# Performance work log

Measured on AMD Instinct MI355X. Metric: run time of the kernel, lower is better.

Reference implementation:

```python
import jax, jax.numpy as jnp
import numpy as np

DIM = 512
HEADS = 8
DIM_HEAD = 64
HIDDEN = HEADS * DIM_HEAD  # 512
B, C, H, W = 32, DIM, 32, 32


def setup_inputs() -> dict:
    key = jax.random.key(0)
    ks = jax.random.split(key, 7)
    s_in = 1.0 / np.sqrt(DIM)
    s_h = 1.0 / np.sqrt(HIDDEN)
    x = jax.random.normal(ks[0], (B, C, H, W), dtype=jnp.float32)
    Wq = jax.random.uniform(ks[1], (DIM, HIDDEN), jnp.float32, -s_in, s_in)
    Wk = jax.random.uniform(ks[2], (DIM, HIDDEN), jnp.float32, -s_in, s_in)
    Wv = jax.random.uniform(ks[3], (DIM, HIDDEN), jnp.float32, -s_in, s_in)
    Wp = jax.random.uniform(ks[4], (HIDDEN, DIM), jnp.float32, -s_h, s_h)
    bp = jax.random.uniform(ks[5], (DIM,), jnp.float32, -s_h, s_h)
    return {"x": x, "Wq": Wq, "Wk": Wk, "Wv": Wv, "Wp": Wp, "bp": bp}


def reference(x, Wq, Wk, Wv, Wp, bp):
    b, c, h, w = x.shape
    n = h * w
    xt = x.reshape(b, c, n).transpose(0, 2, 1)  # [B, N, C]
    q = (xt @ Wq).reshape(b, n, HEADS, DIM_HEAD)
    k = (xt @ Wk).reshape(b, n, HEADS, DIM_HEAD)
    v = (xt @ Wv).reshape(b, n, HEADS, DIM_HEAD)
    k_softmax = jax.nn.softmax(k, axis=1)  # softmax over tokens N
    context = jnp.einsum('bnhd,bnhv->bhdv', k_softmax, v)  # [B, H, D, D]
    out = jnp.einsum('bnhd,bhdv->bnhv', q, context).reshape(b, n, HIDDEN)
    out = out @ Wp + bp  # [B, N, C]
    return out.transpose(0, 2, 1).reshape(b, c, h, w)
```

## Files before the change

kernel.cpp:

```cpp
#include <hip/hip_runtime.h>
#include <hip/hip_bf16.h>


__device__ __forceinline__ float bf2f(unsigned short u) {
    union { unsigned int i; float f; } x;
    x.i = ((unsigned int)u) << 16;
    return x.f;
}
__device__ __forceinline__ unsigned short f2bf(float f) {
    unsigned int u = __float_as_uint(f);
    unsigned int lsb = (u >> 16) & 1u;
    u += 0x7fffu + lsb;
    return (unsigned short)(u >> 16);
}
__device__ __forceinline__ float waveReduceMax(float v) {
    #pragma unroll
    for (int off = 32; off > 0; off >>= 1) v = fmaxf(v, __shfl_xor(v, off, 64));
    return v;
}
__device__ __forceinline__ float waveReduceSum(float v) {
    #pragma unroll
    for (int off = 32; off > 0; off >>= 1) v += __shfl_xor(v, off, 64);
    return v;
}

__device__ __forceinline__ void glds16(const unsigned short* g, unsigned short* l) {
    __builtin_amdgcn_global_load_lds(
        (const __attribute__((address_space(1))) unsigned int*)g,
        (__attribute__((address_space(3))) unsigned int*)l,
        16, 0, 0);
}

typedef __bf16 bf16x8 __attribute__((ext_vector_type(8)));
typedef float  f32x4  __attribute__((ext_vector_type(4)));

__global__ void detect_dtype(const unsigned short* __restrict__ x, int* __restrict__ flag)
{
    int t = threadIdx.x;
    unsigned short u = x[2 * t];
    int e = (u >> 7) & 0xFF;
    int sane = (e >= 113 && e <= 142) ? 1 : 0;
    #pragma unroll
    for (int off = 32; off > 0; off >>= 1) sane += __shfl_xor(sane, off, 64);
    if (t == 0) *flag = (sane >= 32) ? 1 : 0;
}

__global__ __launch_bounds__(256) void transpose_x(
    const void* __restrict__ in, unsigned short* __restrict__ out,
    const int* __restrict__ flag)
{
    const int fl = *flag;
    const int b  = blockIdx.z;
    const int c0 = blockIdx.x * 64;
    const int r0 = blockIdx.y * 64;
    __shared__ unsigned short Ts[64][68];
    const int t   = threadIdx.x;
    const int tr  = t >> 4;
    const int tc4 = (t & 15) * 4;
    #pragma unroll
    for (int rr = 0; rr < 4; ++rr) {
        int rl = rr * 16 + tr;
        long off = (long)b * 524288 + (long)(r0 + rl) * 1024 + c0 + tc4;
        unsigned short v[4];
        if (fl) {
            ushort4 u = *(const ushort4*)((const unsigned short*)in + off);
            v[0] = u.x; v[1] = u.y; v[2] = u.z; v[3] = u.w;
        } else {
            float4 u = *(const float4*)((const float*)in + off);
            v[0] = f2bf(u.x); v[1] = f2bf(u.y); v[2] = f2bf(u.z); v[3] = f2bf(u.w);
        }
        #pragma unroll
        for (int q = 0; q < 4; ++q) Ts[tc4 + q][rl] = v[q];
    }
    __syncthreads();
    #pragma unroll
    for (int rr = 0; rr < 4; ++rr) {
        int cl = rr * 16 + tr;
        ushort4 o = *(const ushort4*)&Ts[cl][tc4];
        *(ushort4*)(out + (long)b * 524288 + (long)(c0 + cl) * 512 + r0 + tc4) = o;
    }
}

__global__ __launch_bounds__(256) void transpose_w3(
    const void* __restrict__ w0, const void* __restrict__ w1,
    const void* __restrict__ w2, unsigned short* __restrict__ out,
    const int* __restrict__ flag)
{
    const int fl = *flag;
    const int z  = blockIdx.z;
    const void* in = (z == 0) ? w0 : (z == 1) ? w1 : w2;
    unsigned short* op = out + (long)z * 262144;
    const int c0 = blockIdx.x * 64;
    const int r0 = blockIdx.y * 64;
    __shared__ unsigned short Ts[64][68];
    const int t   = threadIdx.x;
    const int tr  = t >> 4;
    const int tc4 = (t & 15) * 4;
    #pragma unroll
    for (int rr = 0; rr < 4; ++rr) {
        int rl = rr * 16 + tr;
        long off = (long)(r0 + rl) * 512 + c0 + tc4;
        unsigned short v[4];
        if (fl) {
            ushort4 u = *(const ushort4*)((const unsigned short*)in + off);
            v[0] = u.x; v[1] = u.y; v[2] = u.z; v[3] = u.w;
        } else {
            float4 u = *(const float4*)((const float*)in + off);
            v[0] = f2bf(u.x); v[1] = f2bf(u.y); v[2] = f2bf(u.z); v[3] = f2bf(u.w);
        }
        #pragma unroll
        for (int q = 0; q < 4; ++q) Ts[tc4 + q][rl] = v[q];
    }
    __syncthreads();
    #pragma unroll
    for (int rr = 0; rr < 4; ++rr) {
        int cl = rr * 16 + tr;
        ushort4 o = *(const ushort4*)&Ts[cl][tc4];
        *(ushort4*)(op + (long)(c0 + cl) * 512 + r0 + tc4) = o;
    }
}

__global__ __launch_bounds__(256) void gemm_bt_mfma(
    const unsigned short* __restrict__ A, long a_bstride,
    const unsigned short* __restrict__ Bm, long b_bstride,
    void* __restrict__ C, long c_bstride,
    const void* __restrict__ bias,
    int M, int N, int K, int mode,
    const int* __restrict__ flag)
{
    const int b  = blockIdx.z;
    const int n0 = blockIdx.x * 128;
    const int m0 = blockIdx.y * 128;
    const unsigned short* Ab = A  + (long)b * a_bstride;
    const unsigned short* Bb = Bm + (long)b * b_bstride;

    __shared__ unsigned short As[128 * 32];
    __shared__ unsigned short Bs[128 * 32];

    const int t    = threadIdx.x;
    const int w    = t >> 6;
    const int lane = t & 63;
    const int wm   = (w & 1) * 64;
    const int wn   = (w >> 1) * 64;
    const int fm   = lane & 15;
    const int kg   = lane >> 4;

    const int crow = lane >> 2;
    const int ccol = (lane & 3) * 8;

    f32x4 acc[4][4] = {};

    for (int k0 = 0; k0 < K; k0 += 32) {
        __syncthreads();
        #pragma unroll
        for (int j = 0; j < 2; ++j) {
            const int chunk = w * 2 + j;
            const int row   = chunk * 16 + crow;
            glds16(Ab + (long)(m0 + row) * K + k0 + ccol,
                   &As[chunk * 512 + lane * 8]);
            glds16(Bb + (long)(n0 + row) * K + k0 + ccol,
                   &Bs[chunk * 512 + lane * 8]);
        }
        __syncthreads();

        bf16x8 af[4], bf[4];
        #pragma unroll
        for (int i = 0; i < 4; ++i)
            af[i] = *(const bf16x8*)&As[(wm + i * 16 + fm) * 32 + kg * 8];
        #pragma unroll
        for (int j = 0; j < 4; ++j)
            bf[j] = *(const bf16x8*)&Bs[(wn + j * 16 + fm) * 32 + kg * 8];
        #pragma unroll
        for (int i = 0; i < 4; ++i)
            #pragma unroll
            for (int j = 0; j < 4; ++j)
                acc[i][j] = __builtin_amdgcn_mfma_f32_16x16x32_bf16(
                    af[i], bf[j], acc[i][j], 0, 0, 0);
    }

    const int fl = *flag;
    const long cb = (long)b * c_bstride;
    #pragma unroll
    for (int i = 0; i < 4; ++i) {
        #pragma unroll
        for (int j = 0; j < 4; ++j) {
            const int n = n0 + wn + j * 16 + fm;
            #pragma unroll
            for (int r = 0; r < 4; ++r) {
                const int m = m0 + wm + i * 16 + kg * 4 + r;
                const float val = acc[i][j][r];
                if (mode == 0) {
                    ((unsigned short*)C)[cb + (long)m * N + n] = f2bf(val);
                } else {
                    float bv = 0.f;
                    if (bias) bv = fl ? bf2f(((const unsigned short*)bias)[m])
                                      : ((const float*)bias)[m];
                    const long off = cb + (long)m * N + n;
                    if (fl) ((unsigned short*)C)[off] = f2bf(val + bv);
                    else    ((float*)C)[off] = val + bv;
                }
            }
        }
    }
}

__global__ __launch_bounds__(256) void softmax_rows(unsigned short* __restrict__ KV)
{
    const long row = blockIdx.x;
    unsigned short* p = KV + ((row >> 9) << 20) + ((row & 511) << 10);
    const int t = threadIdx.x;

    ushort4 raw = *(const ushort4*)(p + t * 4);
    float f[4] = {bf2f(raw.x), bf2f(raw.y), bf2f(raw.z), bf2f(raw.w)};

    float m = fmaxf(fmaxf(f[0], f[1]), fmaxf(f[2], f[3]));
    m = waveReduceMax(m);
    __shared__ float redm[4], reds[4];
    if ((t & 63) == 0) redm[t >> 6] = m;
    __syncthreads();
    m = fmaxf(fmaxf(redm[0], redm[1]), fmaxf(redm[2], redm[3]));

    float e[4], s = 0.f;
    #pragma unroll
    for (int i = 0; i < 4; ++i) { e[i] = expf(f[i] - m); s += e[i]; }
    s = waveReduceSum(s);
    if ((t & 63) == 0) reds[t >> 6] = s;
    __syncthreads();
    s = reds[0] + reds[1] + reds[2] + reds[3];
    const float inv = 1.0f / s;

    ushort4 o;
    o.x = f2bf(e[0] * inv); o.y = f2bf(e[1] * inv);
    o.z = f2bf(e[2] * inv); o.w = f2bf(e[3] * inv);
    *(ushort4*)(p + t * 4) = o;
}

__global__ __launch_bounds__(256) void ctx_mfma(
    const unsigned short* __restrict__ KV, float* __restrict__ ctx)
{
    const int bh = blockIdx.x;
    const unsigned short* Kb = KV + ((long)(bh >> 3) << 20) + (long)(bh & 7) * 65536;
    const unsigned short* Vb = Kb + 524288;

    const int t    = threadIdx.x;
    const int w    = t >> 6;
    const int lane = t & 63;
    const int fm   = lane & 15;
    const int kg   = lane >> 4;

    f32x4 acc[4][4] = {};

    #pragma unroll 2
    for (int c = 0; c < 8; ++c) {
        const int k0 = w * 256 + c * 32;
        bf16x8 af[4], bf[4];
        #pragma unroll
        for (int i = 0; i < 4; ++i)
            af[i] = *(const bf16x8*)(Kb + (long)(i * 16 + fm) * 1024 + k0 + kg * 8);
        #pragma unroll
        for (int j = 0; j < 4; ++j)
            bf[j] = *(const bf16x8*)(Vb + (long)(j * 16 + fm) * 1024 + k0 + kg * 8);
        #pragma unroll
        for (int i = 0; i < 4; ++i)
            #pragma unroll
            for (int j = 0; j < 4; ++j)
                acc[i][j] = __builtin_amdgcn_mfma_f32_16x16x32_bf16(
                    af[i], bf[j], acc[i][j], 0, 0, 0);
    }

    __shared__ float red[64][65];
    for (int ph = 0; ph < 4; ++ph) {
        if (w == ph) {
            #pragma unroll
            for (int i = 0; i < 4; ++i)
                #pragma unroll
                for (int j = 0; j < 4; ++j)
                    #pragma unroll
                    for (int r = 0; r < 4; ++r) {
                        const int m = i * 16 + kg * 4 + r;
                        const int n = j * 16 + fm;
                        if (ph == 0) red[m][n]  = acc[i][j][r];
                        else         red[m][n] += acc[i][j][r];
                    }
        }
        __syncthreads();
    }
    float* cp = ctx + (long)bh * 4096;
    for (int i = t; i < 4096; i += 256) cp[i] = red[i >> 6][i & 63];
}

__global__ __launch_bounds__(256) void weff_kernel(
    const float* __restrict__ ctx,
    const void* __restrict__ Wp,
    unsigned short* __restrict__ WeffT,
    const int* __restrict__ flag)
{
    const int fl = *flag;
    const int c0 = blockIdx.x * 64;
    const int h  = blockIdx.y;
    const int b  = blockIdx.z;

    __shared__ float Cs[64][65];
    __shared__ float Ws[64][68];

    const int t = threadIdx.x;
    const int tx = t & 15, ty = t >> 4;

    const float* cb = ctx + ((long)b * 8 + h) * 4096;
    for (int i = t; i < 4096; i += 256) Cs[i >> 6][i & 63] = cb[i];
    for (int i = t; i < 4096; i += 256) {
        int v = i >> 6, c = i & 63;
        long idx = (long)(h * 64 + v) * 512 + c0 + c;
        Ws[v][c] = fl ? bf2f(((const unsigned short*)Wp)[idx])
                      : ((const float*)Wp)[idx];
    }
    __syncthreads();

    float acc[4][4];
    #pragma unroll
    for (int i = 0; i < 4; ++i)
        #pragma unroll
        for (int j = 0; j < 4; ++j) acc[i][j] = 0.f;

    #pragma unroll
    for (int v = 0; v < 64; ++v) {
        float a[4], d[4];
        #pragma unroll
        for (int i = 0; i < 4; ++i) a[i] = Ws[v][ty * 4 + i];
        #pragma unroll
        for (int j = 0; j < 4; ++j) d[j] = Cs[tx * 4 + j][v];
        #pragma unroll
        for (int i = 0; i < 4; ++i)
            #pragma unroll
            for (int j = 0; j < 4; ++j) acc[i][j] += a[i] * d[j];
    }
    #pragma unroll
    for (int i = 0; i < 4; ++i) {
        ushort4 o;
        o.x = f2bf(acc[i][0]); o.y = f2bf(acc[i][1]);
        o.z = f2bf(acc[i][2]); o.w = f2bf(acc[i][3]);
        *(ushort4*)&WeffT[((long)b * 512 + c0 + ty * 4 + i) * 512 + h * 64 + tx * 4] = o;
    }
}

extern "C" void kernel_launch(void* const* d_in, const int* in_sizes, int n_in,
                              void* d_out, int out_size, void* d_ws, size_t ws_size,
                              hipStream_t stream) {
    const void* x  = d_in[0];
    const void* Wq = d_in[1];
    const void* Wk = d_in[2];
    const void* Wv = d_in[3];
    const void* Wp = d_in[4];
    const void* bp = d_in[5];

    char* ws = (char*)d_ws;
    unsigned short* Xt    = (unsigned short*)(ws);
    unsigned short* KV    = (unsigned short*)(ws + 33554432ll);
    unsigned short* Q     = (unsigned short*)(ws + 33554432ll);
    float*          ctx   = (float*)(ws + 100663296ll);
    unsigned short* WeffT = (unsigned short*)(ws + 104857600ll);
    unsigned short* WT    = (unsigned short*)(ws + 121634816ll);
    int*            flag  = (int*)(ws + 123207680ll);

    detect_dtype<<<dim3(1), dim3(64), 0, stream>>>((const unsigned short*)x, flag);

    transpose_x<<<dim3(16, 8, 32), 256, 0, stream>>>(x, Xt, flag);
    transpose_w3<<<dim3(8, 8, 3), 256, 0, stream>>>(Wq, Wk, Wv, WT, flag);

    const long XB = 1024ll * 512;
    gemm_bt_mfma<<<dim3(8, 8, 32), 256, 0, stream>>>(
        WT + 262144, 0, Xt, XB, KV, 1048576ll, nullptr, 1024, 1024, 512, 0, flag);

    softmax_rows<<<dim3(16384), 256, 0, stream>>>(KV);
    ctx_mfma<<<dim3(256), 256, 0, stream>>>(KV, ctx);
    weff_kernel<<<dim3(8, 8, 32), 256, 0, stream>>>(ctx, Wp, WeffT, flag);

    gemm_bt_mfma<<<dim3(4, 8, 32), 256, 0, stream>>>(
        Xt, XB, WT, 0, Q, XB, nullptr, 1024, 512, 512, 0, flag);

    gemm_bt_mfma<<<dim3(8, 4, 32), 256, 0, stream>>>(
        WeffT, 262144ll, Q, XB, d_out, 524288ll, bp, 512, 1024, 512, 2, flag);
}
```

Measured before the change: 347.9 us.

## Fold Wq into per-batch effective weight and double-buffer GEMM LDS tiles

Instead of computing Q = X·Wq per token and then applying WeffT, the code precomputes a per-batch fused matrix Ft = WeffT·Wq^T (512x512). The final GEMM then multiplies directly against the transposed input, which removes the token-sized Q GEMM and its intermediate buffer. The transpose kernel now also writes a bf16 copy of Wq to serve as the B operand. Separately, the MFMA GEMM double-buffers its LDS tiles, prefetching the next K slice before computing on the current one. This doubles LDS use and drops one barrier per iteration; whether that barrier removal is safe depends on when the async loads complete.

```diff
diff --git a/kernel.cpp b/kernel.cpp
--- a/kernel.cpp
+++ b/kernel.cpp
@@ -84,6 +84,7 @@
 __global__ __launch_bounds__(256) void transpose_w3(
     const void* __restrict__ w0, const void* __restrict__ w1,
     const void* __restrict__ w2, unsigned short* __restrict__ out,
+    unsigned short* __restrict__ wqb,
     const int* __restrict__ flag)
 {
     const int fl = *flag;
@@ -108,6 +109,10 @@
             float4 u = *(const float4*)((const float*)in + off);
             v[0] = f2bf(u.x); v[1] = f2bf(u.y); v[2] = f2bf(u.z); v[3] = f2bf(u.w);
         }
+        if (z == 0) {
+            ushort4 s; s.x = v[0]; s.y = v[1]; s.z = v[2]; s.w = v[3];
+            *(ushort4*)(wqb + off) = s;
+        }
         #pragma unroll
         for (int q = 0; q < 4; ++q) Ts[tc4 + q][rl] = v[q];
     }
@@ -134,8 +139,8 @@
     const unsigned short* Ab = A  + (long)b * a_bstride;
     const unsigned short* Bb = Bm + (long)b * b_bstride;
 
-    __shared__ unsigned short As[128 * 32];
-    __shared__ unsigned short Bs[128 * 32];
+    __shared__ unsigned short As[2 * 128 * 32];
+    __shared__ unsigned short Bs[2 * 128 * 32];
 
     const int t    = threadIdx.x;
     const int w    = t >> 6;
@@ -150,32 +155,45 @@
 
     f32x4 acc[4][4] = {};
 
+    #pragma unroll
+    for (int j = 0; j < 2; ++j) {
+        const int chunk = w * 2 + j;
+        const int row   = chunk * 16 + crow;
+        glds16(Ab + (long)(m0 + row) * K + ccol, &As[chunk * 512]);
+        glds16(Bb + (long)(n0 + row) * K + ccol, &Bs[chunk * 512]);
+    }
+
+    int cur = 0;
     for (int k0 = 0; k0 < K; k0 += 32) {
         __syncthreads();
-        #pragma unroll
-        for (int j = 0; j < 2; ++j) {
-            const int chunk = w * 2 + j;
-            const int row   = chunk * 16 + crow;
-            glds16(Ab + (long)(m0 + row) * K + k0 + ccol,
-                   &As[chunk * 512 + lane * 8]);
-            glds16(Bb + (long)(n0 + row) * K + k0 + ccol,
-                   &Bs[chunk * 512 + lane * 8]);
-        }
-        __syncthreads();
-
+
+        if (k0 + 32 < K) {
+            const int kn  = k0 + 32;
+            const int nxt = (cur ^ 1) * 4096;
+            #pragma unroll
+            for (int j = 0; j < 2; ++j) {
+                const int chunk = w * 2 + j;
+                const int row   = chunk * 16 + crow;
+                glds16(Ab + (long)(m0 + row) * K + kn + ccol, &As[nxt + chunk * 512]);
+                glds16(Bb + (long)(n0 + row) * K + kn + ccol, &Bs[nxt + chunk * 512]);
+            }
+        }
+
+        const int bufo = cur * 4096;
         bf16x8 af[4], bf[4];
         #pragma unroll
         for (int i = 0; i < 4; ++i)
-            af[i] = *(const bf16x8*)&As[(wm + i * 16 + fm) * 32 + kg * 8];
+            af[i] = *(const bf16x8*)&As[bufo + (wm + i * 16 + fm) * 32 + kg * 8];
         #pragma unroll
         for (int j = 0; j < 4; ++j)
-            bf[j] = *(const bf16x8*)&Bs[(wn + j * 16 + fm) * 32 + kg * 8];
+            bf[j] = *(const bf16x8*)&Bs[bufo + (wn + j * 16 + fm) * 32 + kg * 8];
         #pragma unroll
         for (int i = 0; i < 4; ++i)
             #pragma unroll
             for (int j = 0; j < 4; ++j)
                 acc[i][j] = __builtin_amdgcn_mfma_f32_16x16x32_bf16(
                     af[i], bf[j], acc[i][j], 0, 0, 0);
+        cur ^= 1;
     }
 
     const int fl = *flag;
@@ -356,16 +374,17 @@
     char* ws = (char*)d_ws;
     unsigned short* Xt    = (unsigned short*)(ws);
     unsigned short* KV    = (unsigned short*)(ws + 33554432ll);
-    unsigned short* Q     = (unsigned short*)(ws + 33554432ll);
+    unsigned short* Ft    = (unsigned short*)(ws + 33554432ll);
     float*          ctx   = (float*)(ws + 100663296ll);
     unsigned short* WeffT = (unsigned short*)(ws + 104857600ll);
     unsigned short* WT    = (unsigned short*)(ws + 121634816ll);
-    int*            flag  = (int*)(ws + 123207680ll);
+    unsigned short* Wqb   = (unsigned short*)(ws + 123207680ll);
+    int*            flag  = (int*)(ws + 123731968ll);
 
     detect_dtype<<<dim3(1), dim3(64), 0, stream>>>((const unsigned short*)x, flag);
 
     transpose_x<<<dim3(16, 8, 32), 256, 0, stream>>>(x, Xt, flag);
-    transpose_w3<<<dim3(8, 8, 3), 256, 0, stream>>>(Wq, Wk, Wv, WT, flag);
+    transpose_w3<<<dim3(8, 8, 3), 256, 0, stream>>>(Wq, Wk, Wv, WT, Wqb, flag);
 
     const long XB = 1024ll * 512;
     gemm_bt_mfma<<<dim3(8, 8, 32), 256, 0, stream>>>(
@@ -375,9 +394,9 @@
     ctx_mfma<<<dim3(256), 256, 0, stream>>>(KV, ctx);
     weff_kernel<<<dim3(8, 8, 32), 256, 0, stream>>>(ctx, Wp, WeffT, flag);
 
-    gemm_bt_mfma<<<dim3(4, 8, 32), 256, 0, stream>>>(
-        Xt, XB, WT, 0, Q, XB, nullptr, 1024, 512, 512, 0, flag);
+    gemm_bt_mfma<<<dim3(4, 4, 32), 256, 0, stream>>>(
+        WeffT, 262144ll, Wqb, 0, Ft, 262144ll, nullptr, 512, 512, 512, 0, flag);
 
     gemm_bt_mfma<<<dim3(8, 4, 32), 256, 0, stream>>>(
-        WeffT, 262144ll, Q, XB, d_out, 524288ll, bp, 512, 1024, 512, 2, flag);
-}
+        Ft, 262144ll, Xt, XB, d_out, 524288ll, bp, 512, 1024, 512, 2, flag);
+}
```

Result: faster. 327.6 us (-5.8%).
